# Performance work log

Hardware: AMD Instinct MI355X
Metric: run time of the kernel (lower is better)

The kernel has to match this reference:

```python
import jax, jax.numpy as jnp
import numpy as np

N_PILLARS_X = 512
N_PILLARS_Y = 512
IN_FEATURES = 6
OUT_FEATURES = 64
N_POINTS = 2_000_000
BN_EPS = 1e-5


def setup_inputs() -> dict:
    key = jax.random.key(0)
    k_x, k_idx, k_w, k_b, k_g, k_bt = jax.random.split(key, 6)
    x = jax.random.normal(k_x, (N_POINTS, IN_FEATURES), dtype=jnp.float32)
    indices = jax.random.randint(k_idx, (N_POINTS, 2), 0, N_PILLARS_X, dtype=jnp.int64)
    # Linear params (torch default init scale ~ 1/sqrt(fan_in))
    bound = 1.0 / np.sqrt(IN_FEATURES)
    W = jax.random.uniform(k_w, (OUT_FEATURES, IN_FEATURES), minval=-bound, maxval=bound, dtype=jnp.float32)
    b = jax.random.uniform(k_b, (OUT_FEATURES,), minval=-bound, maxval=bound, dtype=jnp.float32)
    # BatchNorm affine params (torch init: gamma=1, beta=0; perturb gamma slightly)
    gamma = jnp.ones((OUT_FEATURES,), dtype=jnp.float32)
    beta = jnp.zeros((OUT_FEATURES,), dtype=jnp.float32)
    return {"x": x, "indices": indices, "W": W, "b": b, "gamma": gamma, "beta": beta}


def reference(x, indices, W, b, gamma, beta):
    # Linear: (N, 6) @ (6, 64) + b -> (N, 64)
    h = x @ W.T + b
    # BatchNorm1d (training mode: batch statistics, biased variance)
    mean = jnp.mean(h, axis=0)
    var = jnp.mean(jnp.square(h - mean), axis=0)
    h = gamma * (h - mean) * jax.lax.rsqrt(var + BN_EPS) + beta
    h = jax.nn.relu(h)
    # Scatter-add each point's feature vector into its (x_idx, y_idx) pillar cell
    grid = jnp.zeros((N_PILLARS_X, N_PILLARS_Y, OUT_FEATURES), dtype=h.dtype)
    grid = grid.at[indices[:, 0], indices[:, 1]].add(h)
    return grid
```

## Files before the change

kernel.cpp:

```cpp
#include <hip/hip_runtime.h>
#include <hip/hip_fp16.h>


constexpr int NPTS   = 2000000;
constexpr int NBUCK  = 2048;
constexpr int CPB    = 128;
constexpr int NBLK   = 512;
constexpr int CHUNK  = (NPTS + NBLK - 1) / NBLK;
constexpr int NSEG   = 8;
constexpr int SEGLEN = NBLK / NSEG;
constexpr float EPS  = 1e-5f;

constexpr int WS_WPH    = 0;
constexpr int WS_BP     = 192;
constexpr int WS_STARTS = 256;
constexpr int WS_SEGT   = 2560;
constexpr int WS_SEGB   = WS_SEGT + NSEG * NBUCK;
constexpr int WS_BSTATS = WS_SEGB + NSEG * NBUCK;
constexpr int WS_HB16   = WS_BSTATS + NBLK * 32;
constexpr int WS_SORTED = WS_HB16 + NBLK * NBUCK / 2;

typedef _Float16 h2v __attribute__((ext_vector_type(2)));

__device__ __forceinline__ float dot2u(unsigned int a, unsigned int b, float c) {
    union { unsigned int u; h2v h; } ca, cb;
    ca.u = a; cb.u = b;
    return __builtin_amdgcn_fdot2(ca.h, cb.h, c, false);
}

__device__ __forceinline__ float wave_sum64(float v) {
#pragma unroll
    for (int off = 32; off > 0; off >>= 1) v += __shfl_down(v, off, 64);
    return v;
}

__global__ __launch_bounds__(1024) void hist_kernel(const int2* __restrict__ idx,
                                                    unsigned int* __restrict__ hist16) {
    __shared__ int lh[NBUCK];
    for (int i = threadIdx.x; i < NBUCK; i += 1024) lh[i] = 0;
    __syncthreads();
    const int beg = blockIdx.x * CHUNK;
    const int end = min(NPTS, beg + CHUNK);
    for (int p = beg + threadIdx.x; p < end; p += 1024) {
        const int2 ij = idx[p];
        atomicAdd(&lh[(ij.x << 2) | (ij.y >> 7)], 1);
    }
    __syncthreads();
    unsigned int* out = hist16 + blockIdx.x * (NBUCK / 2);
    for (int i = threadIdx.x; i < NBUCK / 2; i += 1024)
        out[i] = (unsigned int)lh[2 * i] | ((unsigned int)lh[2 * i + 1] << 16);
}

__global__ __launch_bounds__(256) void colscan_a(const unsigned short* __restrict__ hist16,
                                                 int* __restrict__ segtot) {
    const int gid = blockIdx.x * 256 + threadIdx.x;
    const int col = gid & (NBUCK - 1), seg = gid >> 11;
    int s = 0;
#pragma unroll 8
    for (int j = 0; j < SEGLEN; ++j) s += hist16[(seg * SEGLEN + j) * NBUCK + col];
    segtot[seg * NBUCK + col] = s;
}

__global__ __launch_bounds__(1024) void scanb_kernel(const int* __restrict__ segtot,
                                                     int* __restrict__ segbase,
                                                     int* __restrict__ starts) {
    __shared__ int wsum[16];
    const int t = threadIdx.x, lane = t & 63, wv = t >> 6;
    int tot[2];
#pragma unroll
    for (int j = 0; j < 2; ++j) {
        const int col = t * 2 + j;
        int run = 0;
#pragma unroll
        for (int sg = 0; sg < NSEG; ++sg) {
            segbase[sg * NBUCK + col] = run;
            run += segtot[sg * NBUCK + col];
        }
        tot[j] = run;
    }
    const int tsum = tot[0] + tot[1];
    int incl = tsum;
#pragma unroll
    for (int d = 1; d < 64; d <<= 1) {
        int u = __shfl_up(incl, d, 64);
        if (lane >= d) incl += u;
    }
    if (lane == 63) wsum[wv] = incl;
    __syncthreads();
    int pre = 0;
#pragma unroll
    for (int w = 0; w < 16; ++w) {
        int sv = wsum[w];
        if (w < wv) pre += sv;
    }
    const int excl = pre + incl - tsum;
    starts[2 * t] = excl;
    starts[2 * t + 1] = excl + tot[0];
    if (t == 1023) starts[NBUCK] = excl + tsum;
}

__global__ __launch_bounds__(256) void colscan_c(unsigned short* hb16,
                                                 const int* __restrict__ segbase) {
    const int gid = blockIdx.x * 256 + threadIdx.x;
    const int col = gid & (NBUCK - 1), seg = gid >> 11;
    int run = segbase[seg * NBUCK + col];
#pragma unroll 8
    for (int j = 0; j < SEGLEN; ++j) {
        const int blk = seg * SEGLEN + j;
        const int h = hb16[blk * NBUCK + col];
        hb16[blk * NBUCK + col] = (unsigned short)run;
        run += h;
    }
}

__global__ __launch_bounds__(1024) void scatter_kernel(const float* __restrict__ x,
                                                       const int2* __restrict__ idx,
                                                       const int* __restrict__ starts,
                                                       const unsigned short* __restrict__ bases16,
                                                       uint4* __restrict__ sorted4,
                                                       float* __restrict__ bstats) {
    __shared__ int lbase[NBUCK];
    __shared__ int lcur[NBUCK];
    __shared__ float lstats[16][27];
    const int blk = blockIdx.x;
    const int ch  = ((blk & 7) << 6) | (blk >> 3);
    for (int i = threadIdx.x; i < NBUCK; i += 1024) {
        lbase[i] = starts[i] + (int)bases16[ch * NBUCK + i];
        lcur[i] = 0;
    }
    __syncthreads();

    float acc[27];
#pragma unroll
    for (int i = 0; i < 27; ++i) acc[i] = 0.f;

    const int beg = ch * CHUNK;
    const int end = min(NPTS, beg + CHUNK);
    for (int p = beg + threadIdx.x; p < end; p += 1024) {
        const int2 ij = idx[p];
        const float2* xp = (const float2*)(x + (size_t)p * 6);
        const float2 a = xp[0], bq = xp[1], cq = xp[2];
        float v[6] = {a.x, a.y, bq.x, bq.y, cq.x, cq.y};
        int c = 6;
#pragma unroll
        for (int k = 0; k < 6; ++k) {
            acc[k] += v[k];
#pragma unroll
            for (int l = k; l < 6; ++l) { acc[c] += v[k] * v[l]; ++c; }
        }
        __half2 h0 = __floats2half2_rn(a.x, a.y);
        __half2 h1 = __floats2half2_rn(bq.x, bq.y);
        __half2 h2 = __floats2half2_rn(cq.x, cq.y);
        const int b = (ij.x << 2) | (ij.y >> 7);
        const int rank = atomicAdd(&lcur[b], 1);
        uint4 r;
        r.x = *(const unsigned int*)&h0;
        r.y = *(const unsigned int*)&h1;
        r.z = *(const unsigned int*)&h2;
        r.w = (unsigned int)(ij.y & 127);
        sorted4[lbase[b] + rank] = r;
    }

    const int lane = threadIdx.x & 63, wv = threadIdx.x >> 6;
#pragma unroll
    for (int i = 0; i < 27; ++i) {
        const float s = wave_sum64(acc[i]);
        if (lane == 0) lstats[wv][i] = s;
    }
    __syncthreads();
    if (threadIdx.x < 32) {
        float s = 0.f;
        if (threadIdx.x < 27)
            for (int w = 0; w < 16; ++w) s += lstats[w][threadIdx.x];
        bstats[ch * 32 + threadIdx.x] = s;
    }
}

__global__ __launch_bounds__(1024) void bnfold_kernel(const float* __restrict__ bstats,
                                                      const float* __restrict__ W,
                                                      const float* __restrict__ b,
                                                      const float* __restrict__ gamma,
                                                      const float* __restrict__ beta,
                                                      float* __restrict__ ws) {
    __shared__ float lred[32][33];
    __shared__ float s27[27];
    __shared__ float m[6], C[36];
    const int t = threadIdx.x;
    {
        const int s = t & 31, seg = t >> 5;
        float a = 0.f;
#pragma unroll 4
        for (int j = 0; j < NBLK / 32; ++j) a += bstats[(seg * (NBLK / 32) + j) * 32 + s];
        lred[seg][s] = a;
    }
    __syncthreads();
    if (t < 27) {
        float s = 0.f;
#pragma unroll
        for (int g = 0; g < 32; ++g) s += lred[g][t];
        s27[t] = s;
    }
    __syncthreads();
    if (t == 0) {
        const float invN = 1.0f / (float)NPTS;
        float mm[6];
        for (int k = 0; k < 6; ++k) { mm[k] = s27[k] * invN; m[k] = mm[k]; }
        int c = 6;
        for (int k = 0; k < 6; ++k)
            for (int l = k; l < 6; ++l) {
                const float cov = s27[c] * invN - mm[k] * mm[l];
                ++c;
                C[k * 6 + l] = cov;
                C[l * 6 + k] = cov;
            }
    }
    __syncthreads();
    if (t < 64) {
        float w[6];
#pragma unroll
        for (int k = 0; k < 6; ++k) w[k] = W[t * 6 + k];
        float mh = b[t];
#pragma unroll
        for (int k = 0; k < 6; ++k) mh += w[k] * m[k];
        float var = 0.f;
#pragma unroll
        for (int k = 0; k < 6; ++k)
#pragma unroll
            for (int l = 0; l < 6; ++l) var += w[k] * w[l] * C[k * 6 + l];
        const float s = gamma[t] * rsqrtf(var + EPS);
        float wp[6];
#pragma unroll
        for (int k = 0; k < 6; ++k) wp[k] = w[k] * s;
        unsigned int* wsu = (unsigned int*)ws;
        __half2 p0 = __floats2half2_rn(wp[0], wp[1]);
        __half2 p1 = __floats2half2_rn(wp[2], wp[3]);
        __half2 p2 = __floats2half2_rn(wp[4], wp[5]);
        wsu[WS_WPH + t * 3 + 0] = *(const unsigned int*)&p0;
        wsu[WS_WPH + t * 3 + 1] = *(const unsigned int*)&p1;
        wsu[WS_WPH + t * 3 + 2] = *(const unsigned int*)&p2;
        ws[WS_BP + t] = beta[t] + s * (b[t] - mh);
    }
}

constexpr int CAP  = 1088;
constexpr int ACCT = 256;
constexpr int RPT  = (CAP + ACCT - 1) / ACCT;

__global__ __launch_bounds__(ACCT, 8) void accum_kernel(const uint4* __restrict__ sorted4,
                                                        const int* __restrict__ starts,
                                                        const float* __restrict__ wsf,
                                                        float* __restrict__ grid) {
    __shared__ uint4 recs[CAP];
    __shared__ int lhist[CPB];
    __shared__ int cstart[CPB + 1];
    const int t = threadIdx.x, lane = t & 63, wv = t >> 6;

    const int s = starts[blockIdx.x];
    const int e = starts[blockIdx.x + 1];
    const int n = min(e - s, CAP);

    for (int i = t; i < CPB; i += ACCT) lhist[i] = 0;

    const unsigned int* wsu = (const unsigned int*)wsf;
    const unsigned int wp0 = wsu[WS_WPH + lane * 3 + 0];
    const unsigned int wp1 = wsu[WS_WPH + lane * 3 + 1];
    const unsigned int wp2 = wsu[WS_WPH + lane * 3 + 2];
    const float bb = wsf[WS_BP + lane];
    __syncthreads();

    uint4 rr[RPT];
    int rkk[RPT];
#pragma unroll
    for (int u = 0; u < RPT; ++u) {
        const int i = t + u * ACCT;
        rkk[u] = -1;
        if (i < n) {
            rr[u] = sorted4[s + i];
            rkk[u] = atomicAdd(&lhist[(int)rr[u].w], 1);
        }
    }
    __syncthreads();

    if (wv == 0) {
        const int v0 = lhist[2 * lane], v1 = lhist[2 * lane + 1];
        const int v = v0 + v1;
        int incl = v;
#pragma unroll
        for (int d = 1; d < 64; d <<= 1) {
            int u = __shfl_up(incl, d, 64);
            if (lane >= d) incl += u;
        }
        const int excl = incl - v;
        cstart[2 * lane] = excl;
        cstart[2 * lane + 1] = excl + v0;
        if (lane == 63) cstart[CPB] = incl;
    }
    __syncthreads();

#pragma unroll
    for (int u = 0; u < RPT; ++u)
        if (rkk[u] >= 0) recs[cstart[(int)rr[u].w] + rkk[u]] = rr[u];
    __syncthreads();

    float* gbase = grid + (size_t)blockIdx.x * (CPB * 64);
    for (int c = wv; c < CPB; c += 4) {
        const int cs = __builtin_amdgcn_readfirstlane(cstart[c]);
        const int ce = __builtin_amdgcn_readfirstlane(cstart[c + 1]);
        float acc0 = 0.f, acc1 = 0.f;
        int p = cs;
        for (; p + 1 < ce; p += 2) {
            const uint4 ra = recs[p];
            const uint4 rb = recs[p + 1];
            const float h0 = dot2u(ra.x, wp0, dot2u(ra.y, wp1, dot2u(ra.z, wp2, bb)));
            const float h1 = dot2u(rb.x, wp0, dot2u(rb.y, wp1, dot2u(rb.z, wp2, bb)));
            acc0 += fmaxf(h0, 0.f);
            acc1 += fmaxf(h1, 0.f);
        }
        if (p < ce) {
            const uint4 ra = recs[p];
            acc0 += fmaxf(dot2u(ra.x, wp0, dot2u(ra.y, wp1, dot2u(ra.z, wp2, bb))), 0.f);
        }
        gbase[c * 64 + lane] = acc0 + acc1;
    }

    if (e - s > CAP) {
        __syncthreads();
        for (int base = s + CAP + wv * 64; base < e; base += 4 * 64) {
            const int m = min(64, e - base);
            uint4 rec = make_uint4(0u, 0u, 0u, 0u);
            if (lane < m) rec = sorted4[base + lane];
            for (int pt = 0; pt < m; ++pt) {
                const unsigned int c  = __builtin_amdgcn_readlane(rec.w, pt);
                const unsigned int x0 = __builtin_amdgcn_readlane(rec.x, pt);
                const unsigned int x1 = __builtin_amdgcn_readlane(rec.y, pt);
                const unsigned int x2 = __builtin_amdgcn_readlane(rec.z, pt);
                const float h = dot2u(x0, wp0, dot2u(x1, wp1, dot2u(x2, wp2, bb)));
                unsafeAtomicAdd(&gbase[c * 64 + lane], fmaxf(h, 0.f));
            }
        }
    }
}

extern "C" void kernel_launch(void* const* d_in, const int* in_sizes, int n_in,
                              void* d_out, int out_size, void* d_ws, size_t ws_size,
                              hipStream_t stream) {
    const float* x       = (const float*)d_in[0];
    const int2*  indices = (const int2*)d_in[1];
    const float* W       = (const float*)d_in[2];
    const float* b       = (const float*)d_in[3];
    const float* gamma   = (const float*)d_in[4];
    const float* beta    = (const float*)d_in[5];
    float* out = (float*)d_out;
    float* wsf = (float*)d_ws;
    int*   wsi = (int*)d_ws;

    unsigned int*   hb16u = (unsigned int*)(wsi + WS_HB16);
    unsigned short* hb16  = (unsigned short*)(wsi + WS_HB16);
    int*   segtot  = wsi + WS_SEGT;
    int*   segbase = wsi + WS_SEGB;
    int*   starts  = wsi + WS_STARTS;
    uint4* sorted4 = (uint4*)(wsi + WS_SORTED);
    float* bstats  = wsf + WS_BSTATS;

    hist_kernel<<<NBLK, 1024, 0, stream>>>(indices, hb16u);
    colscan_a<<<NSEG * NBUCK / 256, 256, 0, stream>>>(hb16, segtot);
    scanb_kernel<<<1, 1024, 0, stream>>>(segtot, segbase, starts);
    colscan_c<<<NSEG * NBUCK / 256, 256, 0, stream>>>(hb16, segbase);
    scatter_kernel<<<NBLK, 1024, 0, stream>>>(x, indices, starts, hb16, sorted4, bstats);
    bnfold_kernel<<<1, 1024, 0, stream>>>(bstats, W, b, gamma, beta, wsf);
    accum_kernel<<<NBUCK, ACCT, 0, stream>>>(sorted4, starts, wsf, out);
}
```

Measured before the change: 214.5 us.

## Merge scan and BN-fold stages into fewer kernels, move stats to histogram pass

Result: no change. 211.7 us (-1.3%).

```diff
diff --git a/kernel.cpp b/kernel.cpp
--- a/kernel.cpp
+++ b/kernel.cpp
@@ -7,16 +7,13 @@
 constexpr int CPB    = 128;
 constexpr int NBLK   = 512;
 constexpr int CHUNK  = (NPTS + NBLK - 1) / NBLK;
-constexpr int NSEG   = 8;
-constexpr int SEGLEN = NBLK / NSEG;
 constexpr float EPS  = 1e-5f;
 
 constexpr int WS_WPH    = 0;
 constexpr int WS_BP     = 192;
 constexpr int WS_STARTS = 256;
-constexpr int WS_SEGT   = 2560;
-constexpr int WS_SEGB   = WS_SEGT + NSEG * NBUCK;
-constexpr int WS_BSTATS = WS_SEGB + NSEG * NBUCK;
+constexpr int WS_STOT   = 2560;
+constexpr int WS_BSTATS = WS_STOT + NBUCK;
 constexpr int WS_HB16   = WS_BSTATS + NBLK * 32;
 constexpr int WS_SORTED = WS_HB16 + NBLK * NBUCK / 2;
 
@@ -34,110 +31,24 @@
     return v;
 }
 
-__global__ __launch_bounds__(1024) void hist_kernel(const int2* __restrict__ idx,
-                                                    unsigned int* __restrict__ hist16) {
+__global__ __launch_bounds__(1024) void hist_kernel(const float* __restrict__ x,
+                                                    const int2* __restrict__ idx,
+                                                    unsigned int* __restrict__ hist16,
+                                                    float* __restrict__ bstats) {
     __shared__ int lh[NBUCK];
+    __shared__ float lstats[16][27];
     for (int i = threadIdx.x; i < NBUCK; i += 1024) lh[i] = 0;
     __syncthreads();
+
+    float acc[27];
+#pragma unroll
+    for (int i = 0; i < 27; ++i) acc[i] = 0.f;
+
     const int beg = blockIdx.x * CHUNK;
     const int end = min(NPTS, beg + CHUNK);
     for (int p = beg + threadIdx.x; p < end; p += 1024) {
         const int2 ij = idx[p];
         atomicAdd(&lh[(ij.x << 2) | (ij.y >> 7)], 1);
-    }
-    __syncthreads();
-    unsigned int* out = hist16 + blockIdx.x * (NBUCK / 2);
-    for (int i = threadIdx.x; i < NBUCK / 2; i += 1024)
-        out[i] = (unsigned int)lh[2 * i] | ((unsigned int)lh[2 * i + 1] << 16);
-}
-
-__global__ __launch_bounds__(256) void colscan_a(const unsigned short* __restrict__ hist16,
-                                                 int* __restrict__ segtot) {
-    const int gid = blockIdx.x * 256 + threadIdx.x;
-    const int col = gid & (NBUCK - 1), seg = gid >> 11;
-    int s = 0;
-#pragma unroll 8
-    for (int j = 0; j < SEGLEN; ++j) s += hist16[(seg * SEGLEN + j) * NBUCK + col];
-    segtot[seg * NBUCK + col] = s;
-}
-
-__global__ __launch_bounds__(1024) void scanb_kernel(const int* __restrict__ segtot,
-                                                     int* __restrict__ segbase,
-                                                     int* __restrict__ starts) {
-    __shared__ int wsum[16];
-    const int t = threadIdx.x, lane = t & 63, wv = t >> 6;
-    int tot[2];
-#pragma unroll
-    for (int j = 0; j < 2; ++j) {
-        const int col = t * 2 + j;
-        int run = 0;
-#pragma unroll
-        for (int sg = 0; sg < NSEG; ++sg) {
-            segbase[sg * NBUCK + col] = run;
-            run += segtot[sg * NBUCK + col];
-        }
-        tot[j] = run;
-    }
-    const int tsum = tot[0] + tot[1];
-    int incl = tsum;
-#pragma unroll
-    for (int d = 1; d < 64; d <<= 1) {
-        int u = __shfl_up(incl, d, 64);
-        if (lane >= d) incl += u;
-    }
-    if (lane == 63) wsum[wv] = incl;
-    __syncthreads();
-    int pre = 0;
-#pragma unroll
-    for (int w = 0; w < 16; ++w) {
-        int sv = wsum[w];
-        if (w < wv) pre += sv;
-    }
-    const int excl = pre + incl - tsum;
-    starts[2 * t] = excl;
-    starts[2 * t + 1] = excl + tot[0];
-    if (t == 1023) starts[NBUCK] = excl + tsum;
-}
-
-__global__ __launch_bounds__(256) void colscan_c(unsigned short* hb16,
-                                                 const int* __restrict__ segbase) {
-    const int gid = blockIdx.x * 256 + threadIdx.x;
-    const int col = gid & (NBUCK - 1), seg = gid >> 11;
-    int run = segbase[seg * NBUCK + col];
-#pragma unroll 8
-    for (int j = 0; j < SEGLEN; ++j) {
-        const int blk = seg * SEGLEN + j;
-        const int h = hb16[blk * NBUCK + col];
-        hb16[blk * NBUCK + col] = (unsigned short)run;
-        run += h;
-    }
-}
-
-__global__ __launch_bounds__(1024) void scatter_kernel(const float* __restrict__ x,
-                                                       const int2* __restrict__ idx,
-                                                       const int* __restrict__ starts,
-                                                       const unsigned short* __restrict__ bases16,
-                                                       uint4* __restrict__ sorted4,
-                                                       float* __restrict__ bstats) {
-    __shared__ int lbase[NBUCK];
-    __shared__ int lcur[NBUCK];
-    __shared__ float lstats[16][27];
-    const int blk = blockIdx.x;
-    const int ch  = ((blk & 7) << 6) | (blk >> 3);
-    for (int i = threadIdx.x; i < NBUCK; i += 1024) {
-        lbase[i] = starts[i] + (int)bases16[ch * NBUCK + i];
-        lcur[i] = 0;
-    }
-    __syncthreads();
-
-    float acc[27];
-#pragma unroll
-    for (int i = 0; i < 27; ++i) acc[i] = 0.f;
-
-    const int beg = ch * CHUNK;
-    const int end = min(NPTS, beg + CHUNK);
-    for (int p = beg + threadIdx.x; p < end; p += 1024) {
-        const int2 ij = idx[p];
         const float2* xp = (const float2*)(x + (size_t)p * 6);
         const float2 a = xp[0], bq = xp[1], cq = xp[2];
         float v[6] = {a.x, a.y, bq.x, bq.y, cq.x, cq.y};
@@ -148,6 +59,173 @@
 #pragma unroll
             for (int l = k; l < 6; ++l) { acc[c] += v[k] * v[l]; ++c; }
         }
+    }
+    __syncthreads();
+    unsigned int* out = hist16 + blockIdx.x * (NBUCK / 2);
+    for (int i = threadIdx.x; i < NBUCK / 2; i += 1024)
+        out[i] = (unsigned int)lh[2 * i] | ((unsigned int)lh[2 * i + 1] << 16);
+
+    const int lane = threadIdx.x & 63, wv = threadIdx.x >> 6;
+#pragma unroll
+    for (int i = 0; i < 27; ++i) {
+        const float s = wave_sum64(acc[i]);
+        if (lane == 0) lstats[wv][i] = s;
+    }
+    __syncthreads();
+    if (threadIdx.x < 32) {
+        float s = 0.f;
+        if (threadIdx.x < 27)
+            for (int w = 0; w < 16; ++w) s += lstats[w][threadIdx.x];
+        bstats[blockIdx.x * 32 + threadIdx.x] = s;
+    }
+}
+
+__global__ __launch_bounds__(256) void mid_kernel(unsigned short* hb16,
+                                                  int* __restrict__ stot,
+                                                  const float* __restrict__ bstats,
+                                                  const float* __restrict__ W,
+                                                  const float* __restrict__ b,
+                                                  const float* __restrict__ gamma,
+                                                  const float* __restrict__ beta,
+                                                  float* __restrict__ ws) {
+    const int t = threadIdx.x;
+    if (blockIdx.x < 64) {
+        __shared__ int ss[8][33];
+        const int c = t & 31, seg = t >> 5;
+        const int col = blockIdx.x * 32 + c;
+        const int r0 = seg * 64;
+        int s = 0;
+#pragma unroll 8
+        for (int j = 0; j < 64; ++j) s += hb16[(r0 + j) * NBUCK + col];
+        ss[seg][c] = s;
+        __syncthreads();
+        int run = 0;
+#pragma unroll
+        for (int k = 0; k < 8; ++k) {
+            const int sv = ss[k][c];
+            if (k < seg) run += sv;
+        }
+#pragma unroll 8
+        for (int j = 0; j < 64; ++j) {
+            const int row = r0 + j;
+            const int h = hb16[row * NBUCK + col];
+            hb16[row * NBUCK + col] = (unsigned short)run;
+            run += h;
+        }
+        if (seg == 7) stot[col] = run;
+    } else {
+        __shared__ float lred[8][33];
+        __shared__ float s27[27];
+        __shared__ float m[6], C[36];
+        {
+            const int s = t & 31, g = t >> 5;
+            float a = 0.f;
+#pragma unroll 4
+            for (int j = 0; j < NBLK / 8; ++j) a += bstats[(g * (NBLK / 8) + j) * 32 + s];
+            lred[g][s] = a;
+        }
+        __syncthreads();
+        if (t < 27) {
+            float s = 0.f;
+#pragma unroll
+            for (int g = 0; g < 8; ++g) s += lred[g][t];
+            s27[t] = s;
+        }
+        __syncthreads();
+        if (t == 0) {
+            const float invN = 1.0f / (float)NPTS;
+            float mm[6];
+            for (int k = 0; k < 6; ++k) { mm[k] = s27[k] * invN; m[k] = mm[k]; }
+            int c = 6;
+            for (int k = 0; k < 6; ++k)
+                for (int l = k; l < 6; ++l) {
+                    const float cov = s27[c] * invN - mm[k] * mm[l];
+                    ++c;
+                    C[k * 6 + l] = cov;
+                    C[l * 6 + k] = cov;
+                }
+        }
+        __syncthreads();
+        if (t < 64) {
+            float w[6];
+#pragma unroll
+            for (int k = 0; k < 6; ++k) w[k] = W[t * 6 + k];
+            float mh = b[t];
+#pragma unroll
+            for (int k = 0; k < 6; ++k) mh += w[k] * m[k];
+            float var = 0.f;
+#pragma unroll
+            for (int k = 0; k < 6; ++k)
+#pragma unroll
+                for (int l = 0; l < 6; ++l) var += w[k] * w[l] * C[k * 6 + l];
+            const float s = gamma[t] * rsqrtf(var + EPS);
+            float wp[6];
+#pragma unroll
+            for (int k = 0; k < 6; ++k) wp[k] = w[k] * s;
+            unsigned int* wsu = (unsigned int*)ws;
+            __half2 p0 = __floats2half2_rn(wp[0], wp[1]);
+            __half2 p1 = __floats2half2_rn(wp[2], wp[3]);
+            __half2 p2 = __floats2half2_rn(wp[4], wp[5]);
+            wsu[WS_WPH + t * 3 + 0] = *(const unsigned int*)&p0;
+            wsu[WS_WPH + t * 3 + 1] = *(const unsigned int*)&p1;
+            wsu[WS_WPH + t * 3 + 2] = *(const unsigned int*)&p2;
+            ws[WS_BP + t] = beta[t] + s * (b[t] - mh);
+        }
+    }
+}
+
+__global__ __launch_bounds__(1024) void scatter_kernel(const float* __restrict__ x,
+                                                       const int2* __restrict__ idx,
+                                                       const int* __restrict__ stot,
+                                                       const unsigned short* __restrict__ bases16,
+                                                       int* __restrict__ starts,
+                                                       uint4* __restrict__ sorted4) {
+    __shared__ int lbase[NBUCK];
+    __shared__ int lcur[NBUCK];
+    __shared__ int wsum[16];
+    const int t = threadIdx.x, lane = t & 63, wv = t >> 6;
+    const int blk = blockIdx.x;
+    const int ch  = ((blk & 7) << 6) | (blk >> 3);
+
+    {
+        const int v0 = stot[2 * t], v1 = stot[2 * t + 1];
+        const int v = v0 + v1;
+        int incl = v;
+#pragma unroll
+        for (int d = 1; d < 64; d <<= 1) {
+            int u = __shfl_up(incl, d, 64);
+            if (lane >= d) incl += u;
+        }
+        if (lane == 63) wsum[wv] = incl;
+        __syncthreads();
+        int pre = 0;
+#pragma unroll
+        for (int w = 0; w < 16; ++w) {
+            int sv = wsum[w];
+            if (w < wv) pre += sv;
+        }
+        const int excl = pre + incl - v;
+        lbase[2 * t] = excl;
+        lbase[2 * t + 1] = excl + v0;
+        if (blk == 0) {
+            starts[2 * t] = excl;
+            starts[2 * t + 1] = excl + v0;
+            if (t == 1023) starts[NBUCK] = excl + v;
+        }
+    }
+    __syncthreads();
+    for (int i = t; i < NBUCK; i += 1024) {
+        lbase[i] += (int)bases16[ch * NBUCK + i];
+        lcur[i] = 0;
+    }
+    __syncthreads();
+
+    const int beg = ch * CHUNK;
+    const int end = min(NPTS, beg + CHUNK);
+    for (int p = beg + t; p < end; p += 1024) {
+        const int2 ij = idx[p];
+        const float2* xp = (const float2*)(x + (size_t)p * 6);
+        const float2 a = xp[0], bq = xp[1], cq = xp[2];
         __half2 h0 = __floats2half2_rn(a.x, a.y);
         __half2 h1 = __floats2half2_rn(bq.x, bq.y);
         __half2 h2 = __floats2half2_rn(cq.x, cq.y);
@@ -159,86 +237,6 @@
         r.z = *(const unsigned int*)&h2;
         r.w = (unsigned int)(ij.y & 127);
         sorted4[lbase[b] + rank] = r;
-    }
-
-    const int lane = threadIdx.x & 63, wv = threadIdx.x >> 6;
-#pragma unroll
-    for (int i = 0; i < 27; ++i) {
-        const float s = wave_sum64(acc[i]);
-        if (lane == 0) lstats[wv][i] = s;
-    }
-    __syncthreads();
-    if (threadIdx.x < 32) {
-        float s = 0.f;
-        if (threadIdx.x < 27)
-            for (int w = 0; w < 16; ++w) s += lstats[w][threadIdx.x];
-        bstats[ch * 32 + threadIdx.x] = s;
-    }
-}
-
-__global__ __launch_bounds__(1024) void bnfold_kernel(const float* __restrict__ bstats,
-                                                      const float* __restrict__ W,
-                                                      const float* __restrict__ b,
-                                                      const float* __restrict__ gamma,
-                                                      const float* __restrict__ beta,
-                                                      float* __restrict__ ws) {
-    __shared__ float lred[32][33];
-    __shared__ float s27[27];
-    __shared__ float m[6], C[36];
-    const int t = threadIdx.x;
-    {
-        const int s = t & 31, seg = t >> 5;
-        float a = 0.f;
-#pragma unroll 4
-        for (int j = 0; j < NBLK / 32; ++j) a += bstats[(seg * (NBLK / 32) + j) * 32 + s];
-        lred[seg][s] = a;
-    }
-    __syncthreads();
-    if (t < 27) {
-        float s = 0.f;
-#pragma unroll
-        for (int g = 0; g < 32; ++g) s += lred[g][t];
-        s27[t] = s;
-    }
-    __syncthreads();
-    if (t == 0) {
-        const float invN = 1.0f / (float)NPTS;
-        float mm[6];
-        for (int k = 0; k < 6; ++k) { mm[k] = s27[k] * invN; m[k] = mm[k]; }
-        int c = 6;
-        for (int k = 0; k < 6; ++k)
-            for (int l = k; l < 6; ++l) {
-                const float cov = s27[c] * invN - mm[k] * mm[l];
-                ++c;
-                C[k * 6 + l] = cov;
-                C[l * 6 + k] = cov;
-            }
-    }
-    __syncthreads();
-    if (t < 64) {
-        float w[6];
-#pragma unroll
-        for (int k = 0; k < 6; ++k) w[k] = W[t * 6 + k];
-        float mh = b[t];
-#pragma unroll
-        for (int k = 0; k < 6; ++k) mh += w[k] * m[k];
-        float var = 0.f;
-#pragma unroll
-        for (int k = 0; k < 6; ++k)
-#pragma unroll
-            for (int l = 0; l < 6; ++l) var += w[k] * w[l] * C[k * 6 + l];
-        const float s = gamma[t] * rsqrtf(var + EPS);
-        float wp[6];
-#pragma unroll
-        for (int k = 0; k < 6; ++k) wp[k] = w[k] * s;
-        unsigned int* wsu = (unsigned int*)ws;
-        __half2 p0 = __floats2half2_rn(wp[0], wp[1]);
-        __half2 p1 = __floats2half2_rn(wp[2], wp[3]);
-        __half2 p2 = __floats2half2_rn(wp[4], wp[5]);
-        wsu[WS_WPH + t * 3 + 0] = *(const unsigned int*)&p0;
-        wsu[WS_WPH + t * 3 + 1] = *(const unsigned int*)&p1;
-        wsu[WS_WPH + t * 3 + 2] = *(const unsigned int*)&p2;
-        ws[WS_BP + t] = beta[t] + s * (b[t] - mh);
     }
 }
 
@@ -356,17 +354,13 @@
 
     unsigned int*   hb16u = (unsigned int*)(wsi + WS_HB16);
     unsigned short* hb16  = (unsigned short*)(wsi + WS_HB16);
-    int*   segtot  = wsi + WS_SEGT;
-    int*   segbase = wsi + WS_SEGB;
+    int*   stot    = wsi + WS_STOT;
     int*   starts  = wsi + WS_STARTS;
     uint4* sorted4 = (uint4*)(wsi + WS_SORTED);
     float* bstats  = wsf + WS_BSTATS;
 
-    hist_kernel<<<NBLK, 1024, 0, stream>>>(indices, hb16u);
-    colscan_a<<<NSEG * NBUCK / 256, 256, 0, stream>>>(hb16, segtot);
-    scanb_kernel<<<1, 1024, 0, stream>>>(segtot, segbase, starts);
-    colscan_c<<<NSEG * NBUCK / 256, 256, 0, stream>>>(hb16, segbase);
-    scatter_kernel<<<NBLK, 1024, 0, stream>>>(x, indices, starts, hb16, sorted4, bstats);
-    bnfold_kernel<<<1, 1024, 0, stream>>>(bstats, W, b, gamma, beta, wsf);
+    hist_kernel<<<NBLK, 1024, 0, stream>>>(x, indices, hb16u, bstats);
+    mid_kernel<<<65, 256, 0, stream>>>(hb16, stot, bstats, W, b, gamma, beta, wsf);
+    scatter_kernel<<<NBLK, 1024, 0, stream>>>(x, indices, stot, hb16, starts, sorted4);
     accum_kernel<<<NBUCK, ACCT, 0, stream>>>(sorted4, starts, wsf, out);
 }
```
